# Performance work log

Hardware: AMD Instinct MI355X
Metric: run time of the kernel (lower is better)

The kernel has to match this reference:

```python
import jax, jax.numpy as jnp
import numpy as np

B, N = 256, 512
DIM_GRAPH = 256
DIM_DESC = 256
RANK = 64


def setup_inputs() -> dict:
    key = jax.random.key(0)
    ks = jax.random.split(key, 6)
    tokns_k = jax.random.normal(ks[0], (B, DIM_DESC), dtype=jnp.float32)
    H_pad = jax.random.normal(ks[1], (B, N, DIM_GRAPH), dtype=jnp.float32)
    mask = jax.random.randint(ks[2], (B, N), 0, 2).astype(bool)
    mask = mask.at[:, 0].set(True)  # ensure at least one valid node per graph
    # Linear weights, torch convention: y = x @ W.T
    Wq = jax.random.normal(ks[3], (RANK, DIM_DESC), dtype=jnp.float32) / np.sqrt(DIM_DESC)
    Wk = jax.random.normal(ks[4], (RANK, DIM_GRAPH), dtype=jnp.float32) / np.sqrt(DIM_GRAPH)
    Wv = jax.random.normal(ks[5], (DIM_DESC, DIM_GRAPH), dtype=jnp.float32) / np.sqrt(DIM_GRAPH)
    log_scale = jnp.zeros((1,), dtype=jnp.float32)
    return {"tokns_k": tokns_k, "H_pad": H_pad, "mask": mask,
            "Wq": Wq, "Wk": Wk, "Wv": Wv, "log_scale": log_scale}


def reference(tokns_k, H_pad, mask, Wq, Wk, Wv, log_scale):
    q = tokns_k @ Wq.T                                  # [B, r]
    k = jnp.einsum('bnd,rd->bnr', H_pad, Wk)            # [B, N, r]
    scale = jnp.maximum(jnp.exp(log_scale), 0.1)        # clamp(min=0.1)
    scores = jnp.einsum('br,bnr->bn', q, k) / scale     # [B, N]
    neg_inf = jnp.float32(-jnp.inf)
    scores = jnp.where(mask, scores, neg_inf)
    alpha = jax.nn.softmax(scores, axis=-1)             # [B, N]
    v = jnp.einsum('bnd,ed->bne', H_pad, Wv)            # [B, N, dim_desc]
    ctx_k = jnp.einsum('bn,bne->be', alpha, v)          # [B, dim_desc]
    return (alpha, ctx_k)
```

## Files before the change

kernel.cpp:

```cpp
#include <hip/hip_runtime.h>

constexpr int Bc = 256;
constexpr int Nc = 512;
constexpr int Dc = 256;
constexpr int Rc = 64;

constexpr int NT    = 1024;
constexpr int NTEAM = 64;
constexpr int NSTEP = Nc / NTEAM;

typedef float f4 __attribute__((ext_vector_type(4)));

__global__ __launch_bounds__(NT) void fba_fused(
    const float* __restrict__ tokns_k, const float* __restrict__ H_pad,
    const int* __restrict__ mask, const float* __restrict__ Wq,
    const float* __restrict__ Wk, const float* __restrict__ Wv,
    const float* __restrict__ log_scale, float* __restrict__ out)
{
    const int b = blockIdx.x;
    const int t = threadIdx.x;
    const int wave = t >> 6, lane = t & 63, g = lane >> 4, l16 = lane & 15;
    const int team = wave * 4 + g;

    __shared__ float q_s[Rc];
    __shared__ __align__(16) float p_s[Dc];
    __shared__ __align__(16) float hm[NTEAM][Dc];
    __shared__ float l_s[NTEAM];
    __shared__ float pn_s[Nc];
    __shared__ __align__(16) float hbar[Dc];
    __shared__ int   mask_s[Nc];

    if (t < Nc) mask_s[t] = mask[b * Nc + t];

    const float inv_scale = 1.0f / fmaxf(__expf(log_scale[0]), 0.1f);

    {
        const int r = team;
        float acc = 0.0f;
        #pragma unroll
        for (int j = 0; j < 4; ++j) {
            const float4 tk = *(const float4*)(tokns_k + b * Dc + l16 * 4 + j * 64);
            const float4 wq = *(const float4*)(Wq + r * Dc + l16 * 4 + j * 64);
            acc += tk.x * wq.x + tk.y * wq.y + tk.z * wq.z + tk.w * wq.w;
        }
        #pragma unroll
        for (int off = 1; off < 16; off <<= 1) acc += __shfl_xor(acc, off);
        if (l16 == 0) q_s[r] = acc;
    }
    __syncthreads();

    {
        const int rg = t >> 8;
        const int d  = t & 255;
        float acc = 0.0f;
        #pragma unroll
        for (int rr = 0; rr < 16; ++rr) {
            const int r = rg * 16 + rr;
            acc += q_s[r] * Wk[r * Dc + d];
        }
        hm[rg][d] = acc;
    }
    __syncthreads();
    if (t < Dc) p_s[t] = (hm[0][t] + hm[1][t]) + (hm[2][t] + hm[3][t]);
    __syncthreads();

    float4 p4[4];
    #pragma unroll
    for (int j = 0; j < 4; ++j) p4[j] = *(const float4*)(p_s + l16 * 4 + j * 64);

    int actbits = 0;
    #pragma unroll
    for (int k = 0; k < NSTEP; ++k)
        actbits |= (mask_s[k * NTEAM + team] != 0) ? (1 << k) : 0;

    const float* __restrict__ Hb = H_pad + (size_t)b * Nc * Dc;
    float  l_acc = 0.0f;
    float4 h4[4];
    #pragma unroll
    for (int j = 0; j < 4; ++j) h4[j] = make_float4(0.f, 0.f, 0.f, 0.f);

    auto LOADROW = [&](f4 (&x)[4], int nr, bool act) {
        if (act) {
            const float* __restrict__ row = Hb + nr * Dc + l16 * 4;
            #pragma unroll
            for (int j = 0; j < 4; ++j)
                x[j] = __builtin_nontemporal_load((const f4*)(row + j * 64));
        }
    };
    auto PROCROW = [&](const f4 (&x)[4], int nr, bool act) {
        if (!act) {
            if (l16 == 0) pn_s[nr] = 0.0f;
            return;
        }
        float s0 = x[0][0] * p4[0].x + x[0][1] * p4[0].y + x[0][2] * p4[0].z + x[0][3] * p4[0].w;
        float s1 = x[1][0] * p4[1].x + x[1][1] * p4[1].y + x[1][2] * p4[1].z + x[1][3] * p4[1].w;
        float s2 = x[2][0] * p4[2].x + x[2][1] * p4[2].y + x[2][2] * p4[2].z + x[2][3] * p4[2].w;
        float s3 = x[3][0] * p4[3].x + x[3][1] * p4[3].y + x[3][2] * p4[3].z + x[3][3] * p4[3].w;
        float sc = (s0 + s1) + (s2 + s3);
        #pragma unroll
        for (int off = 1; off < 16; off <<= 1) sc += __shfl_xor(sc, off);
        sc *= inv_scale;

        const float pn = __expf(sc);
        if (l16 == 0) pn_s[nr] = pn;
        l_acc += pn;
        #pragma unroll
        for (int j = 0; j < 4; ++j) {
            h4[j].x = fmaf(pn, x[j][0], h4[j].x);
            h4[j].y = fmaf(pn, x[j][1], h4[j].y);
            h4[j].z = fmaf(pn, x[j][2], h4[j].z);
            h4[j].w = fmaf(pn, x[j][3], h4[j].w);
        }
    };

    f4 xa[4], xb[4];
    LOADROW(xa, team, (actbits >> 0) & 1);
    #pragma unroll
    for (int it = 0; it < NSTEP / 2; ++it) {
        const int nrA = it * (2 * NTEAM) + team;
        const int nrB = nrA + NTEAM;
        const bool actA = (actbits >> (2 * it)) & 1;
        const bool actB = (actbits >> (2 * it + 1)) & 1;
        LOADROW(xb, nrB, actB);
        PROCROW(xa, nrA, actA);
        if (it + 1 < NSTEP / 2)
            LOADROW(xa, nrA + 2 * NTEAM, (actbits >> (2 * it + 2)) & 1);
        PROCROW(xb, nrB, actB);
    }

    #pragma unroll
    for (int j = 0; j < 4; ++j) *(float4*)(&hm[team][l16 * 4 + j * 64]) = h4[j];
    if (l16 == 0) l_s[team] = l_acc;
    __syncthreads();

    float L = 0.0f;
    #pragma unroll
    for (int p = 0; p < NTEAM; ++p) L += l_s[p];
    const float invL = 1.0f / L;

    if (t < Dc) {
        float hsum = 0.0f;
        #pragma unroll
        for (int p = 0; p < NTEAM; ++p) hsum += hm[p][t];
        hbar[t] = hsum * invL;
    }
    if (t < Nc) out[b * Nc + t] = pn_s[t] * invL;
    __syncthreads();

    float4 hb4[4];
    #pragma unroll
    for (int j = 0; j < 4; ++j) hb4[j] = *(const float4*)(hbar + l16 * 4 + j * 64);
    float* __restrict__ ctx_out = out + (size_t)Bc * Nc + b * Dc;
    #pragma unroll
    for (int step = 0; step < Dc / NTEAM; ++step) {
        const int e = step * NTEAM + team;
        float acc = 0.0f;
        #pragma unroll
        for (int j = 0; j < 4; ++j) {
            const float4 wv = *(const float4*)(Wv + e * Dc + l16 * 4 + j * 64);
            acc += wv.x * hb4[j].x + wv.y * hb4[j].y + wv.z * hb4[j].z + wv.w * hb4[j].w;
        }
        #pragma unroll
        for (int off = 1; off < 16; off <<= 1) acc += __shfl_xor(acc, off);
        if (l16 == 0) ctx_out[e] = acc;
    }
}

extern "C" void kernel_launch(void* const* d_in, const int* in_sizes, int n_in,
                              void* d_out, int out_size, void* d_ws, size_t ws_size,
                              hipStream_t stream) {
    const float* tokns_k   = (const float*)d_in[0];
    const float* H_pad     = (const float*)d_in[1];
    const int*   mask      = (const int*)d_in[2];
    const float* Wq        = (const float*)d_in[3];
    const float* Wk        = (const float*)d_in[4];
    const float* Wv        = (const float*)d_in[5];
    const float* log_scale = (const float*)d_in[6];
    float* out = (float*)d_out;
    (void)d_ws; (void)ws_size;

    fba_fused<<<Bc, NT, 0, stream>>>(tokns_k, H_pad, mask, Wq, Wk, Wv,
                                     log_scale, out);
}
```

Measured before the change: 187.4 us.

## Split node rows across two blocks per batch and merge in a second kernel

Replaces the single fused kernel (one 1024-thread block per batch) with a two-kernel path. The first kernel splits each batch's 512 rows across two 512-thread blocks, giving 512 blocks instead of 256, and uses a triple-buffered row prefetch that overlaps the first loads with the Wk projection. The second kernel merges the partial softmax sums and weighted row sums, normalizes alpha, and applies Wv. It also parallelizes the reduction of per-team partial sums across all threads. The intent is better CU occupancy and load overlap on a bandwidth-bound stream of H, at the cost of an extra launch, workspace round-trips, and a read-modify-write of alpha. Skipping the running max in the softmax, as before, is unchanged.

```diff
diff --git a/kernel.cpp b/kernel.cpp
--- a/kernel.cpp
+++ b/kernel.cpp
@@ -5,11 +5,205 @@
 constexpr int Dc = 256;
 constexpr int Rc = 64;
 
+constexpr int SPLIT2 = 2;
+constexpr int ROWS2  = Nc / SPLIT2;
+constexpr int NT1    = 512;
+constexpr int NTEAM1 = 32;
+constexpr int NSTEP1 = ROWS2 / NTEAM1;
+
+typedef float f4 __attribute__((ext_vector_type(4)));
+
+constexpr size_t WS_L = 0;
+constexpr size_t WS_H = WS_L + (size_t)Bc * SPLIT2;
+constexpr size_t WS_FLOATS = WS_H + (size_t)Bc * SPLIT2 * Dc;
+
+__global__ __launch_bounds__(NT1) void k1_half(
+    const float* __restrict__ tokns_k, const float* __restrict__ H_pad,
+    const int* __restrict__ mask, const float* __restrict__ Wq,
+    const float* __restrict__ Wk, const float* __restrict__ log_scale,
+    float* __restrict__ ws, float* __restrict__ out)
+{
+    const int s = blockIdx.x;
+    const int b = blockIdx.y;
+    const int t = threadIdx.x;
+    const int wave = t >> 6, lane = t & 63, g = lane >> 4, l16 = lane & 15;
+    const int team = wave * 4 + g;
+    const int n0 = s * ROWS2;
+
+    __shared__ float q_s[Rc];
+    __shared__ __align__(16) float hm[NTEAM1][Dc];
+    __shared__ __align__(16) float hq[2][Dc];
+    __shared__ float l_s[NTEAM1];
+    __shared__ float pn_s[ROWS2];
+    __shared__ int   mask_s[ROWS2];
+
+    if (t < ROWS2) mask_s[t] = mask[b * Nc + n0 + t];
+
+    const float inv_scale = 1.0f / fmaxf(__expf(log_scale[0]), 0.1f);
+
+    #pragma unroll
+    for (int step = 0; step < 2; ++step) {
+        const int r = step * NTEAM1 + team;
+        float acc = 0.0f;
+        #pragma unroll
+        for (int j = 0; j < 4; ++j) {
+            const float4 tk = *(const float4*)(tokns_k + b * Dc + l16 * 4 + j * 64);
+            const float4 wq = *(const float4*)(Wq + r * Dc + l16 * 4 + j * 64);
+            acc += tk.x * wq.x + tk.y * wq.y + tk.z * wq.z + tk.w * wq.w;
+        }
+        #pragma unroll
+        for (int off = 1; off < 16; off <<= 1) acc += __shfl_xor(acc, off);
+        if (l16 == 0) q_s[r] = acc;
+    }
+    __syncthreads();
+
+    int actbits = 0;
+    #pragma unroll
+    for (int k = 0; k < NSTEP1; ++k)
+        actbits |= (mask_s[k * NTEAM1 + team] != 0) ? (1 << k) : 0;
+
+    const float* __restrict__ Hb = H_pad + ((size_t)b * Nc + n0) * Dc;
+
+    auto LOADROW = [&](f4 (&x)[4], int nr, bool act) {
+        if (act) {
+            const float* __restrict__ row = Hb + nr * Dc + l16 * 4;
+            #pragma unroll
+            for (int j = 0; j < 4; ++j)
+                x[j] = __builtin_nontemporal_load((const f4*)(row + j * 64));
+        }
+    };
+
+    f4 xbuf[3][4];
+    LOADROW(xbuf[0], 0 * NTEAM1 + team, (actbits >> 0) & 1);
+    LOADROW(xbuf[1], 1 * NTEAM1 + team, (actbits >> 1) & 1);
+
+    {
+        const int rg = t >> 8;
+        const int d  = t & 255;
+        float acc = 0.0f;
+        #pragma unroll
+        for (int rr = 0; rr < 32; ++rr) {
+            const int r = rg * 32 + rr;
+            acc += q_s[r] * Wk[r * Dc + d];
+        }
+        hq[rg][d] = acc;
+    }
+    __syncthreads();
+
+    f4 p4[4];
+    #pragma unroll
+    for (int j = 0; j < 4; ++j)
+        p4[j] = *(const f4*)(&hq[0][l16 * 4 + j * 64]) +
+                *(const f4*)(&hq[1][l16 * 4 + j * 64]);
+
+    float l_acc = 0.0f;
+    f4 h4[4];
+    #pragma unroll
+    for (int j = 0; j < 4; ++j) h4[j] = (f4){0.f, 0.f, 0.f, 0.f};
+
+    auto PROCROW = [&](const f4 (&x)[4], int nr, bool act) {
+        if (!act) {
+            if (l16 == 0) pn_s[nr] = 0.0f;
+            return;
+        }
+        float s0 = x[0][0] * p4[0][0] + x[0][1] * p4[0][1] + x[0][2] * p4[0][2] + x[0][3] * p4[0][3];
+        float s1 = x[1][0] * p4[1][0] + x[1][1] * p4[1][1] + x[1][2] * p4[1][2] + x[1][3] * p4[1][3];
+        float s2 = x[2][0] * p4[2][0] + x[2][1] * p4[2][1] + x[2][2] * p4[2][2] + x[2][3] * p4[2][3];
+        float s3 = x[3][0] * p4[3][0] + x[3][1] * p4[3][1] + x[3][2] * p4[3][2] + x[3][3] * p4[3][3];
+        float sc = (s0 + s1) + (s2 + s3);
+        #pragma unroll
+        for (int off = 1; off < 16; off <<= 1) sc += __shfl_xor(sc, off);
+        sc *= inv_scale;
+
+        const float pn = __expf(sc);
+        if (l16 == 0) pn_s[nr] = pn;
+        l_acc += pn;
+        #pragma unroll
+        for (int j = 0; j < 4; ++j) {
+            h4[j][0] = fmaf(pn, x[j][0], h4[j][0]);
+            h4[j][1] = fmaf(pn, x[j][1], h4[j][1]);
+            h4[j][2] = fmaf(pn, x[j][2], h4[j][2]);
+            h4[j][3] = fmaf(pn, x[j][3], h4[j][3]);
+        }
+    };
+
+    #pragma unroll
+    for (int i = 0; i < NSTEP1; ++i) {
+        if (i + 2 < NSTEP1)
+            LOADROW(xbuf[(i + 2) % 3], (i + 2) * NTEAM1 + team, (actbits >> (i + 2)) & 1);
+        PROCROW(xbuf[i % 3], i * NTEAM1 + team, (actbits >> i) & 1);
+    }
+
+    #pragma unroll
+    for (int j = 0; j < 4; ++j) *(f4*)(&hm[team][l16 * 4 + j * 64]) = h4[j];
+    if (l16 == 0) l_s[team] = l_acc;
+    __syncthreads();
+
+    {
+        const int rg = t >> 8;
+        const int d  = t & 255;
+        float hsum = 0.0f;
+        #pragma unroll
+        for (int pp = 0; pp < 16; ++pp) hsum += hm[rg * 16 + pp][d];
+        hq[rg][d] = hsum;
+    }
+    if (t < ROWS2) out[b * Nc + n0 + t] = pn_s[t];
+    if (t == 0) {
+        float L = 0.0f;
+        #pragma unroll
+        for (int p = 0; p < NTEAM1; ++p) L += l_s[p];
+        ws[WS_L + (size_t)b * SPLIT2 + s] = L;
+    }
+    __syncthreads();
+    if (t < Dc)
+        ws[WS_H + ((size_t)b * SPLIT2 + s) * Dc + t] = hq[0][t] + hq[1][t];
+}
+
+__global__ __launch_bounds__(256) void k2_merge(
+    const float* __restrict__ Wv, const float* __restrict__ ws,
+    float* __restrict__ out)
+{
+    const int b = blockIdx.x;
+    const int t = threadIdx.x;
+    const int wave = t >> 6, lane = t & 63, g = lane >> 4, l16 = lane & 15;
+
+    __shared__ __align__(16) float hbar[Dc];
+
+    const float L = ws[WS_L + (size_t)b * SPLIT2] + ws[WS_L + (size_t)b * SPLIT2 + 1];
+    const float invL = 1.0f / L;
+
+    hbar[t] = (ws[WS_H + ((size_t)b * SPLIT2 + 0) * Dc + t] +
+               ws[WS_H + ((size_t)b * SPLIT2 + 1) * Dc + t]) * invL;
+
+    #pragma unroll
+    for (int i = 0; i < Nc / 256; ++i) {
+        const int idx = b * Nc + i * 256 + t;
+        out[idx] = out[idx] * invL;
+    }
+    __syncthreads();
+
+    float4 hb4[4];
+    #pragma unroll
+    for (int j = 0; j < 4; ++j) hb4[j] = *(const float4*)(hbar + l16 * 4 + j * 64);
+    float* __restrict__ ctx_out = out + (size_t)Bc * Nc + b * Dc;
+    #pragma unroll
+    for (int step = 0; step < 16; ++step) {
+        const int e = step * 16 + wave * 4 + g;
+        float acc = 0.0f;
+        #pragma unroll
+        for (int j = 0; j < 4; ++j) {
+            const float4 wv = *(const float4*)(Wv + e * Dc + l16 * 4 + j * 64);
+            acc += wv.x * hb4[j].x + wv.y * hb4[j].y + wv.z * hb4[j].z + wv.w * hb4[j].w;
+        }
+        #pragma unroll
+        for (int off = 1; off < 16; off <<= 1) acc += __shfl_xor(acc, off);
+        if (l16 == 0) ctx_out[e] = acc;
+    }
+}
+
 constexpr int NT    = 1024;
 constexpr int NTEAM = 64;
 constexpr int NSTEP = Nc / NTEAM;
-
-typedef float f4 __attribute__((ext_vector_type(4)));
 
 __global__ __launch_bounds__(NT) void fba_fused(
     const float* __restrict__ tokns_k, const float* __restrict__ H_pad,
@@ -25,6 +219,7 @@
     __shared__ float q_s[Rc];
     __shared__ __align__(16) float p_s[Dc];
     __shared__ __align__(16) float hm[NTEAM][Dc];
+    __shared__ __align__(16) float hq[4][Dc];
     __shared__ float l_s[NTEAM];
     __shared__ float pn_s[Nc];
     __shared__ __align__(16) float hbar[Dc];
@@ -58,10 +253,10 @@
             const int r = rg * 16 + rr;
             acc += q_s[r] * Wk[r * Dc + d];
         }
-        hm[rg][d] = acc;
-    }
-    __syncthreads();
-    if (t < Dc) p_s[t] = (hm[0][t] + hm[1][t]) + (hm[2][t] + hm[3][t]);
+        hq[rg][d] = acc;
+    }
+    __syncthreads();
+    if (t < Dc) p_s[t] = (hq[0][t] + hq[1][t]) + (hq[2][t] + hq[3][t]);
     __syncthreads();
 
     float4 p4[4];
@@ -138,13 +333,17 @@
     for (int p = 0; p < NTEAM; ++p) L += l_s[p];
     const float invL = 1.0f / L;
 
-    if (t < Dc) {
+    {
+        const int rg = t >> 8;
+        const int d  = t & 255;
         float hsum = 0.0f;
         #pragma unroll
-        for (int p = 0; p < NTEAM; ++p) hsum += hm[p][t];
-        hbar[t] = hsum * invL;
+        for (int pp = 0; pp < 16; ++pp) hsum += hm[rg * 16 + pp][d];
+        hq[rg][d] = hsum;
     }
     if (t < Nc) out[b * Nc + t] = pn_s[t] * invL;
+    __syncthreads();
+    if (t < Dc) hbar[t] = ((hq[0][t] + hq[1][t]) + (hq[2][t] + hq[3][t])) * invL;
     __syncthreads();
 
     float4 hb4[4];
@@ -177,8 +376,15 @@
     const float* Wv        = (const float*)d_in[5];
     const float* log_scale = (const float*)d_in[6];
     float* out = (float*)d_out;
-    (void)d_ws; (void)ws_size;
-
-    fba_fused<<<Bc, NT, 0, stream>>>(tokns_k, H_pad, mask, Wq, Wk, Wv,
-                                     log_scale, out);
+
+    if (ws_size >= WS_FLOATS * sizeof(float)) {
+        float* ws = (float*)d_ws;
+        dim3 grid1(SPLIT2, Bc);
+        k1_half<<<grid1, NT1, 0, stream>>>(tokns_k, H_pad, mask, Wq, Wk,
+                                           log_scale, ws, out);
+        k2_merge<<<Bc, 256, 0, stream>>>(Wv, ws, out);
+    } else {
+        fba_fused<<<Bc, NT, 0, stream>>>(tokns_k, H_pad, mask, Wq, Wk, Wv,
+                                         log_scale, out);
+    }
 }
```

Result: slower. 197.7 us (+5.5%).

## Prefetch first H rows before Wk projection and parallelize final reductions

Applied to the files above, without the earlier changes.

Issues the first two H row loads before the Wk projection so the global memory latency overlaps the q·Wk setup. It also removes one barrier by having every thread sum the four partial projections directly. The 64-way hm reduction is split across all 1024 threads in two stages instead of 256 threads doing 64 adds each. Double buffering now refills xb after it is processed rather than before processing xa. The cost is one extra barrier in the epilogue and more live registers early in the kernel.

```diff
diff --git a/kernel.cpp b/kernel.cpp
--- a/kernel.cpp
+++ b/kernel.cpp
@@ -23,8 +23,8 @@
     const int team = wave * 4 + g;
 
     __shared__ float q_s[Rc];
-    __shared__ __align__(16) float p_s[Dc];
     __shared__ __align__(16) float hm[NTEAM][Dc];
+    __shared__ __align__(16) float hq[4][Dc];
     __shared__ float l_s[NTEAM];
     __shared__ float pn_s[Nc];
     __shared__ __align__(16) float hbar[Dc];
@@ -49,6 +49,26 @@
     }
     __syncthreads();
 
+    int actbits = 0;
+    #pragma unroll
+    for (int k = 0; k < NSTEP; ++k)
+        actbits |= (mask_s[k * NTEAM + team] != 0) ? (1 << k) : 0;
+
+    const float* __restrict__ Hb = H_pad + (size_t)b * Nc * Dc;
+
+    auto LOADROW = [&](f4 (&x)[4], int nr, bool act) {
+        if (act) {
+            const float* __restrict__ row = Hb + nr * Dc + l16 * 4;
+            #pragma unroll
+            for (int j = 0; j < 4; ++j)
+                x[j] = __builtin_nontemporal_load((const f4*)(row + j * 64));
+        }
+    };
+
+    f4 xa[4], xb[4];
+    LOADROW(xa, 0 * NTEAM + team, (actbits >> 0) & 1);
+    LOADROW(xb, 1 * NTEAM + team, (actbits >> 1) & 1);
+
     {
         const int rg = t >> 8;
         const int d  = t & 255;
@@ -58,44 +78,32 @@
             const int r = rg * 16 + rr;
             acc += q_s[r] * Wk[r * Dc + d];
         }
-        hm[rg][d] = acc;
+        hq[rg][d] = acc;
     }
     __syncthreads();
-    if (t < Dc) p_s[t] = (hm[0][t] + hm[1][t]) + (hm[2][t] + hm[3][t]);
-    __syncthreads();
 
-    float4 p4[4];
+    f4 p4[4];
     #pragma unroll
-    for (int j = 0; j < 4; ++j) p4[j] = *(const float4*)(p_s + l16 * 4 + j * 64);
+    for (int j = 0; j < 4; ++j)
+        p4[j] = (*(const f4*)(&hq[0][l16 * 4 + j * 64]) +
+                 *(const f4*)(&hq[1][l16 * 4 + j * 64])) +
+                (*(const f4*)(&hq[2][l16 * 4 + j * 64]) +
+                 *(const f4*)(&hq[3][l16 * 4 + j * 64]));
 
-    int actbits = 0;
+    float l_acc = 0.0f;
+    f4 h4[4];
     #pragma unroll
-    for (int k = 0; k < NSTEP; ++k)
-        actbits |= (mask_s[k * NTEAM + team] != 0) ? (1 << k) : 0;
+    for (int j = 0; j < 4; ++j) h4[j] = (f4){0.f, 0.f, 0.f, 0.f};
 
-    const float* __restrict__ Hb = H_pad + (size_t)b * Nc * Dc;
-    float  l_acc = 0.0f;
-    float4 h4[4];
-    #pragma unroll
-    for (int j = 0; j < 4; ++j) h4[j] = make_float4(0.f, 0.f, 0.f, 0.f);
-
-    auto LOADROW = [&](f4 (&x)[4], int nr, bool act) {
-        if (act) {
-            const float* __restrict__ row = Hb + nr * Dc + l16 * 4;
-            #pragma unroll
-            for (int j = 0; j < 4; ++j)
-                x[j] = __builtin_nontemporal_load((const f4*)(row + j * 64));
-        }
-    };
     auto PROCROW = [&](const f4 (&x)[4], int nr, bool act) {
         if (!act) {
             if (l16 == 0) pn_s[nr] = 0.0f;
             return;
         }
-        float s0 = x[0][0] * p4[0].x + x[0][1] * p4[0].y + x[0][2] * p4[0].z + x[0][3] * p4[0].w;
-        float s1 = x[1][0] * p4[1].x + x[1][1] * p4[1].y + x[1][2] * p4[1].z + x[1][3] * p4[1].w;
-        float s2 = x[2][0] * p4[2].x + x[2][1] * p4[2].y + x[2][2] * p4[2].z + x[2][3] * p4[2].w;
-        float s3 = x[3][0] * p4[3].x + x[3][1] * p4[3].y + x[3][2] * p4[3].z + x[3][3] * p4[3].w;
+        float s0 = x[0][0] * p4[0][0] + x[0][1] * p4[0][1] + x[0][2] * p4[0][2] + x[0][3] * p4[0][3];
+        float s1 = x[1][0] * p4[1][0] + x[1][1] * p4[1][1] + x[1][2] * p4[1][2] + x[1][3] * p4[1][3];
+        float s2 = x[2][0] * p4[2][0] + x[2][1] * p4[2][1] + x[2][2] * p4[2][2] + x[2][3] * p4[2][3];
+        float s3 = x[3][0] * p4[3][0] + x[3][1] * p4[3][1] + x[3][2] * p4[3][2] + x[3][3] * p4[3][3];
         float sc = (s0 + s1) + (s2 + s3);
         #pragma unroll
         for (int off = 1; off < 16; off <<= 1) sc += __shfl_xor(sc, off);
@@ -106,30 +114,29 @@
         l_acc += pn;
         #pragma unroll
         for (int j = 0; j < 4; ++j) {
-            h4[j].x = fmaf(pn, x[j][0], h4[j].x);
-            h4[j].y = fmaf(pn, x[j][1], h4[j].y);
-            h4[j].z = fmaf(pn, x[j][2], h4[j].z);
-            h4[j].w = fmaf(pn, x[j][3], h4[j].w);
+            h4[j][0] = fmaf(pn, x[j][0], h4[j][0]);
+            h4[j][1] = fmaf(pn, x[j][1], h4[j][1]);
+            h4[j][2] = fmaf(pn, x[j][2], h4[j][2]);
+            h4[j][3] = fmaf(pn, x[j][3], h4[j][3]);
         }
     };
 
-    f4 xa[4], xb[4];
-    LOADROW(xa, team, (actbits >> 0) & 1);
     #pragma unroll
     for (int it = 0; it < NSTEP / 2; ++it) {
         const int nrA = it * (2 * NTEAM) + team;
         const int nrB = nrA + NTEAM;
         const bool actA = (actbits >> (2 * it)) & 1;
         const bool actB = (actbits >> (2 * it + 1)) & 1;
-        LOADROW(xb, nrB, actB);
         PROCROW(xa, nrA, actA);
         if (it + 1 < NSTEP / 2)
             LOADROW(xa, nrA + 2 * NTEAM, (actbits >> (2 * it + 2)) & 1);
         PROCROW(xb, nrB, actB);
+        if (it + 1 < NSTEP / 2)
+            LOADROW(xb, nrB + 2 * NTEAM, (actbits >> (2 * it + 3)) & 1);
     }
 
     #pragma unroll
-    for (int j = 0; j < 4; ++j) *(float4*)(&hm[team][l16 * 4 + j * 64]) = h4[j];
+    for (int j = 0; j < 4; ++j) *(f4*)(&hm[team][l16 * 4 + j * 64]) = h4[j];
     if (l16 == 0) l_s[team] = l_acc;
     __syncthreads();
 
@@ -138,18 +145,22 @@
     for (int p = 0; p < NTEAM; ++p) L += l_s[p];
     const float invL = 1.0f / L;
 
-    if (t < Dc) {
+    {
+        const int rg = t >> 8;
+        const int d  = t & 255;
         float hsum = 0.0f;
         #pragma unroll
-        for (int p = 0; p < NTEAM; ++p) hsum += hm[p][t];
-        hbar[t] = hsum * invL;
+        for (int pp = 0; pp < 16; ++pp) hsum += hm[rg * 16 + pp][d];
+        hq[rg][d] = hsum;
     }
     if (t < Nc) out[b * Nc + t] = pn_s[t] * invL;
     __syncthreads();
+    if (t < Dc) hbar[t] = ((hq[0][t] + hq[1][t]) + (hq[2][t] + hq[3][t])) * invL;
+    __syncthreads();
 
-    float4 hb4[4];
+    f4 hb4[4];
     #pragma unroll
-    for (int j = 0; j < 4; ++j) hb4[j] = *(const float4*)(hbar + l16 * 4 + j * 64);
+    for (int j = 0; j < 4; ++j) hb4[j] = *(const f4*)(hbar + l16 * 4 + j * 64);
     float* __restrict__ ctx_out = out + (size_t)Bc * Nc + b * Dc;
     #pragma unroll
     for (int step = 0; step < Dc / NTEAM; ++step) {
@@ -157,8 +168,8 @@
         float acc = 0.0f;
         #pragma unroll
         for (int j = 0; j < 4; ++j) {
-            const float4 wv = *(const float4*)(Wv + e * Dc + l16 * 4 + j * 64);
-            acc += wv.x * hb4[j].x + wv.y * hb4[j].y + wv.z * hb4[j].z + wv.w * hb4[j].w;
+            const f4 wv = *(const f4*)(Wv + e * Dc + l16 * 4 + j * 64);
+            acc += wv[0] * hb4[j][0] + wv[1] * hb4[j][1] + wv[2] * hb4[j][2] + wv[3] * hb4[j][3];
         }
         #pragma unroll
         for (int off = 1; off < 16; off <<= 1) acc += __shfl_xor(acc, off);
```

Measured after the change: 187.7 us. Within noise of the previous version (+0.2%).
